# Kernel tuning notes

Hardware: AMD Instinct MI355X
Metric: run time of the kernel (lower is better)

The kernel has to match this reference:

```python
import jax, jax.numpy as jnp
import numpy as np

N, E1, E2, P, H = 4096, 131072, 131072, 65536, 128
ROLE_VOCAB, ROLE_DIM, IDX_VOCAB, IDX_DIM = 8, 16, 1024, 8


def _lin_init(key, fan_in, fan_out):
    k1, k2 = jax.random.split(key)
    bound = 1.0 / np.sqrt(fan_in)
    W = jax.random.uniform(k1, (fan_in, fan_out), jnp.float32, -bound, bound)
    b = jax.random.uniform(k2, (fan_out,), jnp.float32, -bound, bound)
    return W, b


def setup_inputs() -> dict:
    key = jax.random.key(0)
    ks = jax.random.split(key, 24)
    d = {}
    d["block_features"] = jax.random.normal(ks[0], (N, 16), jnp.float32)
    d["role_ids"] = jax.random.randint(ks[1], (N,), 0, ROLE_VOCAB)
    d["b2b_src"] = jax.random.randint(ks[2], (E1,), 0, N)
    d["b2b_dst"] = jax.random.randint(ks[3], (E1,), 0, N)
    d["b2b_w"] = jax.random.uniform(ks[4], (E1,), jnp.float32)
    d["p2b_pin"] = jax.random.randint(ks[5], (E2,), 0, P)
    d["p2b_block"] = jax.random.randint(ks[6], (E2,), 0, N)
    d["p2b_w"] = jax.random.uniform(ks[7], (E2,), jnp.float32)
    d["pins_pos"] = jax.random.normal(ks[8], (P, 2), jnp.float32)
    d["area_targets"] = jax.random.uniform(ks[9], (N,), jnp.float32)
    # parameters
    d["role_emb"] = jax.random.normal(ks[10], (ROLE_VOCAB, ROLE_DIM), jnp.float32)
    d["idx_emb"] = jax.random.normal(ks[11], (IDX_VOCAB, IDX_DIM), jnp.float32)
    d["in_W1"], d["in_b1"] = _lin_init(ks[12], 16 + IDX_DIM + ROLE_DIM, H)
    d["in_W2"], d["in_b2"] = _lin_init(ks[13], H, H)
    d["b2b_W1"], d["b2b_b1"] = _lin_init(ks[14], 2 * H + 1, H)
    d["b2b_W2"], d["b2b_b2"] = _lin_init(ks[15], H, H)
    d["p2b_W1"], d["p2b_b1"] = _lin_init(ks[16], H + 3, H)
    d["p2b_W2"], d["p2b_b2"] = _lin_init(ks[17], H, H)
    d["self_W"], d["self_b"] = _lin_init(ks[18], H, H)
    d["ln_g"] = jnp.ones((H,), jnp.float32)
    d["ln_b"] = jnp.zeros((H,), jnp.float32)
    d["gp_W1"], d["gp_b1"] = _lin_init(ks[19], 2 * H, H)
    d["gp_W2"], d["gp_b2"] = _lin_init(ks[20], H, H)
    return d


def _mlp2(x, W1, b1, W2, b2):
    return jax.nn.relu(x @ W1 + b1) @ W2 + b2


def _forward(block_features, role_ids, b2b_src, b2b_dst, b2b_w, p2b_pin, p2b_block,
             p2b_w, pins_pos, area_targets, role_emb, idx_emb, in_W1, in_b1, in_W2,
             in_b2, b2b_W1, b2b_b1, b2b_W2, b2b_b2, p2b_W1, p2b_b1, p2b_W2, p2b_b2,
             self_W, self_b, ln_g, ln_b, gp_W1, gp_b1, gp_W2, gp_b2):
    n = block_features.shape[0]
    role_e = role_emb[role_ids]                       # [N, role_dim]
    idx_e = idx_emb[jnp.arange(n) % IDX_VOCAB]        # [N, idx_dim]
    x = jnp.concatenate([block_features, role_e, idx_e], axis=-1)
    h = jax.nn.relu(_mlp2(x, in_W1, in_b1, in_W2, in_b2))  # input_proj ends in ReLU

    # --- b2b messages: two directed messages per undirected edge ---
    max_b2b = jax.lax.stop_gradient(jnp.maximum(jnp.max(jnp.abs(b2b_w)), 1.0))
    w = (b2b_w / max_b2b)[:, None]                    # [E1, 1]
    hi, hj = h[b2b_src], h[b2b_dst]                   # [E1, H]
    m_ij = _mlp2(jnp.concatenate([hi, hj, w], -1), b2b_W1, b2b_b1, b2b_W2, b2b_b2)
    m_ji = _mlp2(jnp.concatenate([hj, hi, w], -1), b2b_W1, b2b_b1, b2b_W2, b2b_b2)
    agg = jnp.zeros_like(h).at[b2b_src].add(m_ij).at[b2b_dst].add(m_ji)

    # --- p2b messages ---
    total_area = jnp.maximum(jnp.sum(area_targets), 1e-6)
    case_scale = jax.lax.stop_gradient(jnp.maximum(jnp.sqrt(total_area), 1e-6))
    max_p2b = jax.lax.stop_gradient(jnp.maximum(jnp.max(jnp.abs(p2b_w)), 1.0))
    pin_feats = jnp.concatenate(
        [pins_pos[p2b_pin] / case_scale, (p2b_w / max_p2b)[:, None]], axis=-1)  # [E2, 3]
    m_p = _mlp2(jnp.concatenate([h[p2b_block], pin_feats], -1),
                p2b_W1, p2b_b1, p2b_W2, p2b_b2)
    agg = agg.at[p2b_block].add(m_p)

    # --- combine + LayerNorm ---
    z = h @ self_W + self_b + agg
    mu = jnp.mean(z, axis=-1, keepdims=True)
    var = jnp.mean(jnp.square(z - mu), axis=-1, keepdims=True)
    block_embeddings = (z - mu) / jnp.sqrt(var + 1e-5) * ln_g + ln_b

    pooled = jnp.concatenate(
        [block_embeddings.mean(axis=0), block_embeddings.max(axis=0)], axis=-1)
    graph_embedding = _mlp2(pooled, gp_W1, gp_b1, gp_W2, gp_b2)
    return block_embeddings, graph_embedding


def reference(block_features, role_ids, b2b_src, b2b_dst, b2b_w, p2b_pin, p2b_block,
              p2b_w, pins_pos, area_targets, role_emb, idx_emb, in_W1, in_b1, in_W2,
              in_b2, b2b_W1, b2b_b1, b2b_W2, b2b_b2, p2b_W1, p2b_b1, p2b_W2, p2b_b2,
              self_W, self_b, ln_g, ln_b, gp_W1, gp_b1, gp_W2, gp_b2):
    block_embeddings, graph_embedding = _forward(
        block_features, role_ids, b2b_src, b2b_dst, b2b_w, p2b_pin, p2b_block,
        p2b_w, pins_pos, area_targets, role_emb, idx_emb, in_W1, in_b1, in_W2,
        in_b2, b2b_W1, b2b_b1, b2b_W2, b2b_b2, p2b_W1, p2b_b1, p2b_W2, p2b_b2,
        self_W, self_b, ln_g, ln_b, gp_W1, gp_b1, gp_W2, gp_b2)
    block_mask = jnp.ones((block_features.shape[0],), dtype=bool)
    return block_embeddings, graph_embedding, block_mask
```

## Files before the change

### kernel.cpp

```cpp
#include <hip/hip_runtime.h>
#include <hip/hip_bf16.h>

#define N_NODES 4096
#define HDIM    128
#define E1      131072
#define E2      131072
#define NMSG_B2B (2 * E1)
#define CAPB    192
#define CAPP    96

#define OFF_PSUM   8
#define OFF_PMAX   136
#define OFF_HB     264
#define OFF_P      (OFF_HB + 262144)
#define OFF_Q      (OFF_P + 524288)
#define OFF_R      (OFF_Q + 524288)
#define OFF_CP     (OFF_R + 524288)
#define OFF_B2H    (OFF_CP + 24576)
#define OFF_B2L    (OFF_B2H + 8192)
#define OFF_P2H    (OFF_B2L + 8192)
#define OFF_P2L    (OFF_P2H + 8192)
#define OFF_SWP    (OFF_P2L + 8192)
#define OFF_IW1    (OFF_SWP + 8192)
#define OFF_IW2    (OFF_IW1 + 4096)
#define OFF_WLAST  (OFF_IW2 + 8192)
#define OFF_PEXTRA (OFF_WLAST + 128)
#define OFF_CNTB   (OFF_PEXTRA + 384)
#define OFF_CNTP   (OFF_CNTB + 4096)
#define OFF_BKB    (OFF_CNTP + 4096)
#define OFF_BKP    (OFF_BKB + 2 * N_NODES * CAPB)
#define WS_FLOATS  (OFF_BKP + 2 * N_NODES * CAPP)

typedef short short8 __attribute__((ext_vector_type(8)));
typedef float f32x4 __attribute__((ext_vector_type(4)));

__device__ __forceinline__ unsigned short f2bf(float f) {
  union { float f; unsigned u; } v; v.f = f;
  unsigned r = v.u + 0x7fffu + ((v.u >> 16) & 1u);
  return (unsigned short)(r >> 16);
}
__device__ __forceinline__ float bf2f(unsigned short h) {
  return __uint_as_float((unsigned)h << 16);
}
__device__ __forceinline__ int il(int c) { return ((c & 63) << 1) | (c >> 6); }

__global__ __launch_bounds__(256) void setup_kernel(const float* __restrict__ b2bw,
                                                    const float* __restrict__ p2bw,
                                                    const float* __restrict__ area,
                                                    const float* __restrict__ bW1,
                                                    const float* __restrict__ bW2,
                                                    const float* __restrict__ pW1,
                                                    const float* __restrict__ pW2,
                                                    const float* __restrict__ sWm,
                                                    const float* __restrict__ iW1,
                                                    const float* __restrict__ iW2,
                                                    float* __restrict__ ws) {
  __shared__ float red[256];
  int b = blockIdx.x, t = threadIdx.x;
  if (b < 32) {
    float m = 0.f;
    for (int i = b * 256 + t; i < E1; i += 32 * 256) m = fmaxf(m, fabsf(b2bw[i]));
    red[t] = m; __syncthreads();
    for (int s = 128; s > 0; s >>= 1) { if (t < s) red[t] = fmaxf(red[t], red[t + s]); __syncthreads(); }
    if (t == 0) atomicMax((unsigned*)&ws[0], __float_as_uint(red[0]));
  } else if (b < 64) {
    float m = 0.f;
    for (int i = (b - 32) * 256 + t; i < E2; i += 32 * 256) m = fmaxf(m, fabsf(p2bw[i]));
    red[t] = m; __syncthreads();
    for (int s = 128; s > 0; s >>= 1) { if (t < s) red[t] = fmaxf(red[t], red[t + s]); __syncthreads(); }
    if (t == 0) atomicMax((unsigned*)&ws[1], __float_as_uint(red[0]));
  } else if (b < 96) {
    float s0 = 0.f;
    for (int i = (b - 64) * 256 + t; i < N_NODES; i += 32 * 256) s0 += area[i];
    red[t] = s0; __syncthreads();
    for (int s = 128; s > 0; s >>= 1) { if (t < s) red[t] += red[t + s]; __syncthreads(); }
    if (t == 0) atomicAdd(&ws[2], red[0]);
  } else if (b == 96) {
    if (t < HDIM) ((int*)ws)[OFF_PMAX + t] = 0x80000000;
    int* cB = (int*)ws + OFF_CNTB;
    for (int i = t; i < 2 * N_NODES; i += 256) cB[i] = 0;
  } else {
    unsigned short* Cp  = (unsigned short*)(ws + OFF_CP);
    unsigned short* B2h = (unsigned short*)(ws + OFF_B2H);
    unsigned short* B2l = (unsigned short*)(ws + OFF_B2L);
    unsigned short* P2h = (unsigned short*)(ws + OFF_P2H);
    unsigned short* P2l = (unsigned short*)(ws + OFF_P2L);
    unsigned short* Swp = (unsigned short*)(ws + OFF_SWP);
    unsigned short* I1p = (unsigned short*)(ws + OFF_IW1);
    unsigned short* I2p = (unsigned short*)(ws + OFF_IW2);
    float* wlast = ws + OFF_WLAST;
    float* pextra = ws + OFF_PEXTRA;
    const int total = 156160;
    for (int x = (b - 97) * 256 + t; x < total; x += 128 * 256) {
      if (x < 49152) {
        int j = x & 7, lane = (x >> 3) & 63, ks = (x >> 9) & 3, nc = x >> 11;
        int col = nc * 16 + (lane & 15), k = ks * 32 + (lane >> 4) * 8 + j;
        float v;
        if (col < 128)      v = bW1[k * 128 + col];
        else if (col < 256) v = bW1[(128 + k) * 128 + (col - 128)];
        else                v = pW1[k * 128 + (col - 256)];
        Cp[x] = f2bf(v);
      } else if (x < 114688) {
        int u = (x - 49152) & 16383, which = (x - 49152) >> 14;
        int j = u & 7, lane = (u >> 3) & 63, ks = (u >> 9) & 3, nt = u >> 11;
        int n = nt * 16 + (lane & 15), k = ks * 32 + (lane >> 4) * 8 + j;
        float v = (which < 2) ? bW2[k * 128 + n] : pW2[k * 128 + n];
        unsigned short hi = f2bf(v);
        unsigned short outv = (which & 1) ? f2bf(v - bf2f(hi)) : hi;
        ((which < 2) ? ((which & 1) ? B2l : B2h) : ((which & 1) ? P2l : P2h))[u] = outv;
      } else if (x < 131072) {
        int u = x - 114688;
        int j = u & 7, lane = (u >> 3) & 63, ks = (u >> 9) & 3, nt = u >> 11;
        int n = nt * 16 + (lane & 15), k = ks * 32 + (lane >> 4) * 8 + j;
        Swp[u] = f2bf(sWm[k * 128 + n]);
      } else if (x < 139264) {
        int u = x - 131072;
        int j = u & 7, lane = (u >> 3) & 63, ks = (u >> 9) & 1, nt = u >> 10;
        int n = nt * 16 + (lane & 15), k = ks * 32 + (lane >> 4) * 8 + j;
        I1p[u] = (k < 40) ? f2bf(iW1[k * 128 + n]) : 0;
      } else if (x < 155648) {
        int u = x - 139264;
        int j = u & 7, lane = (u >> 3) & 63, ks = (u >> 9) & 3, nt = u >> 11;
        int n = nt * 16 + (lane & 15), k = ks * 32 + (lane >> 4) * 8 + j;
        I2p[u] = f2bf(iW2[k * 128 + n]);
      } else if (x < 155776) {
        int c = x - 155648;
        wlast[il(c)] = bW1[256 * 128 + c];
      } else {
        int u = x - 155776;
        int r = u >> 7, c = u & 127;
        pextra[r * 128 + il(c)] = pW1[(128 + r) * 128 + c];
      }
    }
  }
}

__global__ __launch_bounds__(512) void mid_kernel(const int* __restrict__ src,
                                                  const int* __restrict__ dst,
                                                  const int* __restrict__ pblk,
                                                  const int* __restrict__ ppin,
                                                  const float* __restrict__ bwv,
                                                  const float* __restrict__ pwv,
                                                  const float* __restrict__ pins,
                                                  const float* __restrict__ bfeat,
                                                  const int* __restrict__ rid,
                                                  const float* __restrict__ remb,
                                                  const float* __restrict__ iemb,
                                                  const float* __restrict__ ib1,
                                                  const float* __restrict__ ib2,
                                                  const float* __restrict__ bb1,
                                                  const float* __restrict__ pb1,
                                                  float* __restrict__ ws,
                                                  unsigned short* __restrict__ hb) {
  __shared__ __attribute__((aligned(16))) unsigned short xs[16 * 72];
  __shared__ __attribute__((aligned(16))) unsigned short h1s[16 * 136];
  __shared__ __attribute__((aligned(16))) unsigned short hs[16 * 136];
  int tid = threadIdx.x;
  if (blockIdx.x < 768) {
    int i = blockIdx.x * 512 + tid;
    int* cntB = (int*)ws + OFF_CNTB;
    int* cntP = (int*)ws + OFF_CNTP;
    uint2* BKB = (uint2*)((int*)ws + OFF_BKB);
    uint2* BKP = (uint2*)((int*)ws + OFF_BKP);
    if (i < NMSG_B2B) {
      int e = i >> 1, d = i & 1;
      int tg = d ? dst[e] : src[e];
      int o  = d ? src[e] : dst[e];
      int pos = atomicAdd(&cntB[tg], 1);
      if (pos < CAPB) {
        uint2 v; v.x = (unsigned)o; v.y = __float_as_uint(bwv[e]);
        BKB[tg * CAPB + pos] = v;
      }
    } else {
      int e = i - NMSG_B2B;
      int pin = ppin[e];
      int tg = pblk[e];
      int pos = atomicAdd(&cntP[tg], 1);
      if (pos < CAPP) {
        uint2 v;
        v.x = ((unsigned)f2bf(pins[pin * 2 + 1]) << 16) | (unsigned)f2bf(pins[pin * 2]);
        v.y = __float_as_uint(pwv[e]);
        BKP[tg * CAPP + pos] = v;
      }
    }
    return;
  }
  const unsigned short* I1p = (const unsigned short*)(ws + OFF_IW1);
  const unsigned short* I2p = (const unsigned short*)(ws + OFF_IW2);
  const unsigned short* Cp  = (const unsigned short*)(ws + OFF_CP);
  float* P = ws + OFF_P;
  float* Q = ws + OFF_Q;
  float* R = ws + OFF_R;
  int n0 = (blockIdx.x - 768) * 16;
  for (int idx = tid; idx < 1024; idx += 512) {
    int m = idx >> 6, c = idx & 63;
    int n = n0 + m;
    float v = 0.f;
    if (c < 16)      v = bfeat[n * 16 + c];
    else if (c < 32) v = remb[rid[n] * 16 + (c - 16)];
    else if (c < 40) v = iemb[(n & 1023) * 8 + (c - 32)];
    xs[m * 72 + c] = f2bf(v);
  }
  __syncthreads();
  int lane = tid & 63, wv = tid >> 6;
  int l15 = lane & 15, q = lane >> 4;
  f32x4 zero = {0.f, 0.f, 0.f, 0.f};
  f32x4 a1 = zero;
#pragma unroll
  for (int ks = 0; ks < 2; ks++) {
    short8 af = *(const short8*)(&xs[l15 * 72 + ks * 32 + q * 8]);
    short8 bfr = *(const short8*)(I1p + ((wv * 2 + ks) * 64 + lane) * 8);
    a1 = __builtin_amdgcn_mfma_f32_16x16x32_bf16(af, bfr, a1, 0, 0, 0);
  }
  {
    int n = wv * 16 + l15;
    float b = ib1[n];
#pragma unroll
    for (int r = 0; r < 4; r++)
      h1s[(q * 4 + r) * 136 + n] = f2bf(fmaxf(a1[r] + b, 0.f));
  }
  __syncthreads();
  f32x4 a2 = zero;
#pragma unroll
  for (int ks = 0; ks < 4; ks++) {
    short8 af = *(const short8*)(&h1s[l15 * 136 + ks * 32 + q * 8]);
    short8 bfr = *(const short8*)(I2p + ((wv * 4 + ks) * 64 + lane) * 8);
    a2 = __builtin_amdgcn_mfma_f32_16x16x32_bf16(af, bfr, a2, 0, 0, 0);
  }
  {
    int n = wv * 16 + l15;
    float b = ib2[n];
#pragma unroll
    for (int r = 0; r < 4; r++) {
      unsigned short hv = f2bf(fmaxf(a2[r] + b, 0.f));
      hs[(q * 4 + r) * 136 + n] = hv;
      hb[(n0 + q * 4 + r) * 128 + n] = hv;
    }
  }
  __syncthreads();
  f32x4 a3[3];
#pragma unroll
  for (int i = 0; i < 3; i++) a3[i] = zero;
#pragma unroll
  for (int ks = 0; ks < 4; ks++) {
    short8 af = *(const short8*)(&hs[l15 * 136 + ks * 32 + q * 8]);
#pragma unroll
    for (int j = 0; j < 3; j++) {
      short8 bfr = *(const short8*)(Cp + (((3 * wv + j) * 4 + ks) * 64 + lane) * 8);
      a3[j] = __builtin_amdgcn_mfma_f32_16x16x32_bf16(af, bfr, a3[j], 0, 0, 0);
    }
  }
#pragma unroll
  for (int j = 0; j < 3; j++) {
    int col = (3 * wv + j) * 16 + l15;
    int arr = col >> 7, cc = col & 127;
    float bias = (arr == 0) ? bb1[cc] : ((arr == 2) ? pb1[cc] : 0.f);
    float* dstp = (arr == 0) ? P : ((arr == 1) ? Q : R);
    int ic = il(cc);
#pragma unroll
    for (int r = 0; r < 4; r++)
      dstp[(n0 + q * 4 + r) * 128 + ic] = a3[j][r] + bias;
  }
}

__global__ __launch_bounds__(1024) void fused_kernel(const unsigned short* __restrict__ hb,
                                                     const float* __restrict__ sb,
                                                     const float* __restrict__ lng,
                                                     const float* __restrict__ lnb,
                                                     const float* __restrict__ bb2,
                                                     const float* __restrict__ pb2,
                                                     const float* __restrict__ gW1,
                                                     const float* __restrict__ gb1,
                                                     const float* __restrict__ gW2,
                                                     const float* __restrict__ gb2,
                                                     float* __restrict__ ws,
                                                     float* __restrict__ out) {
  __shared__ __attribute__((aligned(16))) unsigned short A[16 * 648];
  __shared__ float partB[16][130];
  __shared__ float partP[16][130];
  __shared__ float zp[2][8 * 128];
  __shared__ float zs[8 * 133];
  __shared__ float muS[8], rsg[8];
  __shared__ float partS[8][16], partQ[8][16];
  __shared__ float psumL[8][128];
  __shared__ int   pmaxL[8][128];
  __shared__ int   isLast;
  int tid = threadIdx.x;
  int n0 = blockIdx.x * 8;
  int lane = tid & 63, wv = tid >> 6;
  const int* cntBp = (const int*)ws + OFF_CNTB;
  const int* cntPp = (const int*)ws + OFF_CNTP;
  if (tid < 128) {
    int m = tid >> 4, o = (tid & 15) * 8;
    *(uint4*)(&A[m * 648 + o]) = *(const uint4*)(hb + (n0 + m) * 128 + o);
  }
  if (tid < 648) {
    int r = tid / 81, o = (tid % 81) * 8;
    *(uint4*)(&A[(8 + r) * 648 + o]) = make_uint4(0u, 0u, 0u, 0u);
  }
  {
    const uint2* BKB = (const uint2*)((const int*)ws + OFF_BKB);
    const uint2* BKP = (const uint2*)((const int*)ws + OFF_BKP);
    const float* Pm = ws + OFF_P;
    const float* Qm = ws + OFF_Q;
    const float* Rm = ws + OFF_R;
    float invb = 1.f / fmaxf(__uint_as_float(((const unsigned*)ws)[0]), 1.f);
    float invp = 1.f / fmaxf(__uint_as_float(((const unsigned*)ws)[1]), 1.f);
    float cs = fmaxf(sqrtf(fmaxf(ws[2], 1e-6f)), 1e-6f);
    float invc = 1.f / cs;
    float2 wlr = *(const float2*)(ws + OFF_WLAST + 2 * lane);
    float2 e0r = *(const float2*)(ws + OFF_PEXTRA + 2 * lane);
    float2 e1r = *(const float2*)(ws + OFF_PEXTRA + 128 + 2 * lane);
    float2 e2r = *(const float2*)(ws + OFF_PEXTRA + 256 + 2 * lane);
    float2 wl = {invb * wlr.x, invb * wlr.y};
    float2 e0 = {invc * e0r.x, invc * e0r.y};
    float2 e1 = {invc * e1r.x, invc * e1r.y};
    float2 e2 = {invp * e2r.x, invp * e2r.y};
    int ln = wv >> 1, hf = wv & 1;
    int node = n0 + ln;
    {
      int cnt = min(cntBp[node], CAPB);
      int mh = cnt >> 1;
      int m = hf ? mh : 0;
      int me = hf ? cnt : mh;
      const uint2* bk = BKB + node * CAPB;
      float2 p = *(const float2*)(Pm + node * 128 + 2 * lane);
      float a0 = 0.f, a1 = 0.f, b0 = 0.f, b1 = 0.f;
      for (; m + 8 <= me; m += 8) {
        uint2 k0 = bk[m],     k1 = bk[m + 1], k2 = bk[m + 2], k3 = bk[m + 3];
        uint2 k4 = bk[m + 4], k5 = bk[m + 5], k6 = bk[m + 6], k7 = bk[m + 7];
        float2 q0 = *(const float2*)(Qm + k0.x * 128 + 2 * lane);
        float2 q1 = *(const float2*)(Qm + k1.x * 128 + 2 * lane);
        float2 q2 = *(const float2*)(Qm + k2.x * 128 + 2 * lane);
        float2 q3 = *(const float2*)(Qm + k3.x * 128 + 2 * lane);
        float2 q4 = *(const float2*)(Qm + k4.x * 128 + 2 * lane);
        float2 q5 = *(const float2*)(Qm + k5.x * 128 + 2 * lane);
        float2 q6 = *(const float2*)(Qm + k6.x * 128 + 2 * lane);
        float2 q7 = *(const float2*)(Qm + k7.x * 128 + 2 * lane);
        float w0 = __uint_as_float(k0.y), w1 = __uint_as_float(k1.y);
        float w2 = __uint_as_float(k2.y), w3 = __uint_as_float(k3.y);
        float w4 = __uint_as_float(k4.y), w5 = __uint_as_float(k5.y);
        float w6 = __uint_as_float(k6.y), w7 = __uint_as_float(k7.y);
        a0 += fmaxf(fmaf(w0, wl.x, p.x) + q0.x, 0.f);
        a1 += fmaxf(fmaf(w0, wl.y, p.y) + q0.y, 0.f);
        b0 += fmaxf(fmaf(w1, wl.x, p.x) + q1.x, 0.f);
        b1 += fmaxf(fmaf(w1, wl.y, p.y) + q1.y, 0.f);
        a0 += fmaxf(fmaf(w2, wl.x, p.x) + q2.x, 0.f);
        a1 += fmaxf(fmaf(w2, wl.y, p.y) + q2.y, 0.f);
        b0 += fmaxf(fmaf(w3, wl.x, p.x) + q3.x, 0.f);
        b1 += fmaxf(fmaf(w3, wl.y, p.y) + q3.y, 0.f);
        a0 += fmaxf(fmaf(w4, wl.x, p.x) + q4.x, 0.f);
        a1 += fmaxf(fmaf(w4, wl.y, p.y) + q4.y, 0.f);
        b0 += fmaxf(fmaf(w5, wl.x, p.x) + q5.x, 0.f);
        b1 += fmaxf(fmaf(w5, wl.y, p.y) + q5.y, 0.f);
        a0 += fmaxf(fmaf(w6, wl.x, p.x) + q6.x, 0.f);
        a1 += fmaxf(fmaf(w6, wl.y, p.y) + q6.y, 0.f);
        b0 += fmaxf(fmaf(w7, wl.x, p.x) + q7.x, 0.f);
        b1 += fmaxf(fmaf(w7, wl.y, p.y) + q7.y, 0.f);
      }
      for (; m < me; m++) {
        uint2 k0 = bk[m];
        float w0 = __uint_as_float(k0.y);
        float2 q0 = *(const float2*)(Qm + k0.x * 128 + 2 * lane);
        a0 += fmaxf(fmaf(w0, wl.x, p.x) + q0.x, 0.f);
        a1 += fmaxf(fmaf(w0, wl.y, p.y) + q0.y, 0.f);
      }
      partB[wv][lane]      = a0 + b0;
      partB[wv][64 + lane] = a1 + b1;
    }
    {
      int cnt = min(cntPp[node], CAPP);
      int mh = cnt >> 1;
      int m = hf ? mh : 0;
      int me = hf ? cnt : mh;
      const uint2* bk = BKP + node * CAPP;
      float2 r = *(const float2*)(Rm + node * 128 + 2 * lane);
      float a0 = 0.f, a1 = 0.f, b0 = 0.f, b1 = 0.f;
      for (; m + 4 <= me; m += 4) {
        uint2 k0 = bk[m], k1 = bk[m + 1], k2 = bk[m + 2], k3 = bk[m + 3];
        float x00 = __uint_as_float((k0.x & 0xFFFFu) << 16);
        float x01 = __uint_as_float(k0.x & 0xFFFF0000u);
        float x02 = __uint_as_float(k0.y);
        float x10 = __uint_as_float((k1.x & 0xFFFFu) << 16);
        float x11 = __uint_as_float(k1.x & 0xFFFF0000u);
        float x12 = __uint_as_float(k1.y);
        float x20 = __uint_as_float((k2.x & 0xFFFFu) << 16);
        float x21 = __uint_as_float(k2.x & 0xFFFF0000u);
        float x22 = __uint_as_float(k2.y);
        float x30 = __uint_as_float((k3.x & 0xFFFFu) << 16);
        float x31 = __uint_as_float(k3.x & 0xFFFF0000u);
        float x32 = __uint_as_float(k3.y);
        a0 += fmaxf(fmaf(x02, e2.x, fmaf(x01, e1.x, fmaf(x00, e0.x, r.x))), 0.f);
        a1 += fmaxf(fmaf(x02, e2.y, fmaf(x01, e1.y, fmaf(x00, e0.y, r.y))), 0.f);
        b0 += fmaxf(fmaf(x12, e2.x, fmaf(x11, e1.x, fmaf(x10, e0.x, r.x))), 0.f);
        b1 += fmaxf(fmaf(x12, e2.y, fmaf(x11, e1.y, fmaf(x10, e0.y, r.y))), 0.f);
        a0 += fmaxf(fmaf(x22, e2.x, fmaf(x21, e1.x, fmaf(x20, e0.x, r.x))), 0.f);
        a1 += fmaxf(fmaf(x22, e2.y, fmaf(x21, e1.y, fmaf(x20, e0.y, r.y))), 0.f);
        b0 += fmaxf(fmaf(x32, e2.x, fmaf(x31, e1.x, fmaf(x30, e0.x, r.x))), 0.f);
        b1 += fmaxf(fmaf(x32, e2.y, fmaf(x31, e1.y, fmaf(x30, e0.y, r.y))), 0.f);
      }
      for (; m < me; m++) {
        uint2 k0 = bk[m];
        float x00 = __uint_as_float((k0.x & 0xFFFFu) << 16);
        float x01 = __uint_as_float(k0.x & 0xFFFF0000u);
        float x02 = __uint_as_float(k0.y);
        a0 += fmaxf(fmaf(x02, e2.x, fmaf(x01, e1.x, fmaf(x00, e0.x, r.x))), 0.f);
        a1 += fmaxf(fmaf(x02, e2.y, fmaf(x01, e1.y, fmaf(x00, e0.y, r.y))), 0.f);
      }
      partP[wv][lane]      = a0 + b0;
      partP[wv][64 + lane] = a1 + b1;
    }
  }
  __syncthreads();
  {
    int r = tid >> 7, c = tid & 127;
    float sb_ = partB[2 * r][c] + partB[2 * r + 1][c];
    float sp_ = partP[2 * r][c] + partP[2 * r + 1][c];
    unsigned short h0 = f2bf(sb_);
    A[r * 648 + 128 + c] = h0;
    A[r * 648 + 256 + c] = f2bf(sb_ - bf2f(h0));
    unsigned short h1v = f2bf(sp_);
    A[r * 648 + 384 + c] = h1v;
    A[r * 648 + 512 + c] = f2bf(sp_ - bf2f(h1v));
  }
  __syncthreads();
  int l15 = lane & 15, q = lane >> 4;
  int ct = wv & 7, half = wv >> 3;
  f32x4 zero = {0.f, 0.f, 0.f, 0.f};
  f32x4 acc = zero;
  const unsigned short* bufs[7] = {
    (const unsigned short*)(ws + OFF_SWP), (const unsigned short*)(ws + OFF_B2H),
    (const unsigned short*)(ws + OFF_B2L), (const unsigned short*)(ws + OFF_B2H),
    (const unsigned short*)(ws + OFF_P2H), (const unsigned short*)(ws + OFF_P2L),
    (const unsigned short*)(ws + OFF_P2H)};
  const int segs[7] = {0, 128, 128, 256, 384, 384, 512};
  int p0 = half ? 4 : 0, p1 = half ? 7 : 4;
  for (int p = p0; p < p1; p++) {
#pragma unroll
    for (int ks = 0; ks < 4; ks++) {
      short8 af = *(const short8*)(&A[l15 * 648 + segs[p] + ks * 32 + q * 8]);
      short8 bfr = *(const short8*)(bufs[p] + ((ct * 4 + ks) * 64 + lane) * 8);
      acc = __builtin_amdgcn_mfma_f32_16x16x32_bf16(af, bfr, acc, 0, 0, 0);
    }
  }
  if (q < 2) {
    int nn = ct * 16 + l15;
#pragma unroll
    for (int r = 0; r < 4; r++)
      zp[half][(q * 4 + r) * 128 + nn] = acc[r];
  }
  __syncthreads();
  {
    int row = tid >> 7, c = tid & 127;
    float cb = (float)cntBp[n0 + row], cp = (float)cntPp[n0 + row];
    zs[row * 133 + c] = zp[0][row * 128 + c] + zp[1][row * 128 + c]
                      + sb[c] + cb * bb2[c] + cp * pb2[c];
  }
  __syncthreads();
  if (tid < 128) {
    int r = tid >> 4, g = tid & 15;
    const float* zr = &zs[r * 133 + g * 8];
    float s = 0.f, s2 = 0.f;
#pragma unroll
    for (int i = 0; i < 8; i++) { float v = zr[i]; s += v; s2 += v * v; }
    partS[r][g] = s; partQ[r][g] = s2;
  }
  __syncthreads();
  if (tid < 8) {
    float s = 0.f, s2 = 0.f;
#pragma unroll
    for (int g = 0; g < 16; g++) { s += partS[tid][g]; s2 += partQ[tid][g]; }
    float m = s * (1.f / 128.f);
    float var = s2 * (1.f / 128.f) - m * m;
    muS[tid] = m;
    rsg[tid] = rsqrtf(fmaxf(var, 0.f) + 1e-5f);
  }
  __syncthreads();
  {
    int row = tid >> 7, c = tid & 127;
    float g = lng[c], b = lnb[c];
    float v = (zs[row * 133 + c] - muS[row]) * rsg[row] * g + b;
    out[(n0 + row) * 128 + c] = v;
    psumL[row][c] = v;
    int e = __float_as_int(v);
    e = e >= 0 ? e : (e ^ 0x7fffffff);
    pmaxL[row][c] = e;
  }
  __syncthreads();
  if (tid < 128) {
    float s = 0.f; int mx = 0x80000000;
#pragma unroll
    for (int g = 0; g < 8; g++) { s += psumL[g][tid]; mx = max(mx, pmaxL[g][tid]); }
    atomicAdd(&ws[OFF_PSUM + tid], s);
    atomicMax(&((int*)ws)[OFF_PMAX + tid], mx);
  }
  if (tid < 8) out[N_NODES * HDIM + HDIM + n0 + tid] = 1.0f;
  __syncthreads();
  if (tid == 0) {
    __threadfence();
    int v = atomicAdd(&((int*)ws)[3], 1);
    isLast = (v == (int)gridDim.x - 1);
  }
  __syncthreads();
  if (!isLast) return;
  __shared__ float pooled[256];
  __shared__ float gpart[8][128];
  __shared__ float g1[128];
  if (tid < 128) {
    pooled[tid] = atomicAdd(&ws[OFF_PSUM + tid], 0.f) * (1.f / (float)N_NODES);
  } else if (tid < 256) {
    int e = atomicAdd(&((int*)ws)[OFF_PMAX + (tid - 128)], 0);
    int bits = e >= 0 ? e : (e ^ 0x7fffffff);
    pooled[tid] = __int_as_float(bits);
  }
  __syncthreads();
  {
    int c = tid & 127, g = tid >> 7;
    float acc2 = 0.f;
#pragma unroll 8
    for (int k = g * 32; k < g * 32 + 32; k++) acc2 += pooled[k] * gW1[k * 128 + c];
    gpart[g][c] = acc2;
  }
  __syncthreads();
  if (tid < 128) {
    float s = gb1[tid];
#pragma unroll
    for (int g = 0; g < 8; g++) s += gpart[g][tid];
    g1[tid] = fmaxf(s, 0.f);
  }
  __syncthreads();
  {
    int c = tid & 127, g = tid >> 7;
    float acc2 = 0.f;
#pragma unroll 8
    for (int k = g * 16; k < g * 16 + 16; k++) acc2 += g1[k] * gW2[k * 128 + c];
    gpart[g][c] = acc2;
  }
  __syncthreads();
  if (tid < 128) {
    float s = gb2[tid];
#pragma unroll
    for (int g = 0; g < 8; g++) s += gpart[g][tid];
    out[N_NODES * HDIM + tid] = s;
  }
}

extern "C" void kernel_launch(void* const* d_in, const int* in_sizes, int n_in,
                              void* d_out, int out_size, void* d_ws, size_t ws_size,
                              hipStream_t stream) {
  const float* bfeat = (const float*)d_in[0];
  const int*   rid   = (const int*)d_in[1];
  const int*   bsrc  = (const int*)d_in[2];
  const int*   bdst  = (const int*)d_in[3];
  const float* bw    = (const float*)d_in[4];
  const int*   ppin  = (const int*)d_in[5];
  const int*   pblk  = (const int*)d_in[6];
  const float* pw    = (const float*)d_in[7];
  const float* pins  = (const float*)d_in[8];
  const float* area  = (const float*)d_in[9];
  const float* remb  = (const float*)d_in[10];
  const float* iemb  = (const float*)d_in[11];
  const float* inW1  = (const float*)d_in[12];
  const float* inb1  = (const float*)d_in[13];
  const float* inW2  = (const float*)d_in[14];
  const float* inb2  = (const float*)d_in[15];
  const float* bW1   = (const float*)d_in[16];
  const float* bb1   = (const float*)d_in[17];
  const float* bW2   = (const float*)d_in[18];
  const float* bb2   = (const float*)d_in[19];
  const float* pW1   = (const float*)d_in[20];
  const float* pb1   = (const float*)d_in[21];
  const float* pW2   = (const float*)d_in[22];
  const float* pb2   = (const float*)d_in[23];
  const float* sW    = (const float*)d_in[24];
  const float* sb    = (const float*)d_in[25];
  const float* lng   = (const float*)d_in[26];
  const float* lnb   = (const float*)d_in[27];
  const float* gW1   = (const float*)d_in[28];
  const float* gb1   = (const float*)d_in[29];
  const float* gW2   = (const float*)d_in[30];
  const float* gb2   = (const float*)d_in[31];

  float* ws  = (float*)d_ws;
  float* out = (float*)d_out;
  unsigned short* hb = (unsigned short*)(ws + OFF_HB);

  hipMemsetAsync(d_ws, 0, 264 * sizeof(float), stream);
  setup_kernel<<<225, 256, 0, stream>>>(bw, pw, area,
                                        bW1, bW2, pW1, pW2, sW, inW1, inW2, ws);
  mid_kernel<<<1024, 512, 0, stream>>>(bsrc, bdst, pblk, ppin, bw, pw, pins,
                                       bfeat, rid, remb, iemb, inb1, inb2, bb1, pb1,
                                       ws, hb);
  fused_kernel<<<512, 1024, 0, stream>>>(hb, sb, lng, lnb, bb2, pb2,
                                         gW1, gb1, gW2, gb2, ws, out);
}
```

Baseline: 204.9 us.

## Split edge aggregation into separate kernel and use full 16-row MFMA tiles

Moves the per-node edge message gather/aggregation out of the fused kernel into a new edge_kernel that writes split-bf16 aggregates to a workspace buffer. The fused kernel then processes 16 nodes per block instead of 8, filling all 16 rows of the MFMA tile instead of zero-padding half of it, which halves the number of blocks and wasted matrix work. The cost is an extra kernel launch and a round trip of the aggregates through global memory.

```diff
diff --git a/kernel.cpp b/kernel.cpp
--- a/kernel.cpp
+++ b/kernel.cpp
@@ -29,7 +29,8 @@
 #define OFF_CNTP   (OFF_CNTB + 4096)
 #define OFF_BKB    (OFF_CNTP + 4096)
 #define OFF_BKP    (OFF_BKB + 2 * N_NODES * CAPB)
-#define WS_FLOATS  (OFF_BKP + 2 * N_NODES * CAPP)
+#define OFF_SB     (OFF_BKP + 2 * N_NODES * CAPP)
+#define WS_FLOATS  (OFF_SB + 524288)
 
 typedef short short8 __attribute__((ext_vector_type(8)));
 typedef float f32x4 __attribute__((ext_vector_type(4)));
@@ -263,6 +264,140 @@
   }
 }
 
+__global__ __launch_bounds__(512) void edge_kernel(float* __restrict__ ws) {
+  __shared__ float partB[8][130];
+  __shared__ float partP[8][130];
+  int tid = threadIdx.x;
+  int lane = tid & 63, wv = tid >> 6;
+  int n0 = blockIdx.x * 4;
+  const int* cntBp = (const int*)ws + OFF_CNTB;
+  const int* cntPp = (const int*)ws + OFF_CNTP;
+  const uint2* BKB = (const uint2*)((const int*)ws + OFF_BKB);
+  const uint2* BKP = (const uint2*)((const int*)ws + OFF_BKP);
+  const float* Pm = ws + OFF_P;
+  const float* Qm = ws + OFF_Q;
+  const float* Rm = ws + OFF_R;
+  float invb = 1.f / fmaxf(__uint_as_float(((const unsigned*)ws)[0]), 1.f);
+  float invp = 1.f / fmaxf(__uint_as_float(((const unsigned*)ws)[1]), 1.f);
+  float cs = fmaxf(sqrtf(fmaxf(ws[2], 1e-6f)), 1e-6f);
+  float invc = 1.f / cs;
+  float2 wlr = *(const float2*)(ws + OFF_WLAST + 2 * lane);
+  float2 e0r = *(const float2*)(ws + OFF_PEXTRA + 2 * lane);
+  float2 e1r = *(const float2*)(ws + OFF_PEXTRA + 128 + 2 * lane);
+  float2 e2r = *(const float2*)(ws + OFF_PEXTRA + 256 + 2 * lane);
+  float2 wl = {invb * wlr.x, invb * wlr.y};
+  float2 e0 = {invc * e0r.x, invc * e0r.y};
+  float2 e1 = {invc * e1r.x, invc * e1r.y};
+  float2 e2 = {invp * e2r.x, invp * e2r.y};
+  int ln = wv >> 1, hf = wv & 1;
+  int node = n0 + ln;
+  {
+    int cnt = min(cntBp[node], CAPB);
+    int mh = cnt >> 1;
+    int m = hf ? mh : 0;
+    int me = hf ? cnt : mh;
+    const uint2* bk = BKB + node * CAPB;
+    float2 p = *(const float2*)(Pm + node * 128 + 2 * lane);
+    float a0 = 0.f, a1 = 0.f, b0 = 0.f, b1 = 0.f;
+    for (; m + 8 <= me; m += 8) {
+      uint2 k0 = bk[m],     k1 = bk[m + 1], k2 = bk[m + 2], k3 = bk[m + 3];
+      uint2 k4 = bk[m + 4], k5 = bk[m + 5], k6 = bk[m + 6], k7 = bk[m + 7];
+      float2 q0 = *(const float2*)(Qm + k0.x * 128 + 2 * lane);
+      float2 q1 = *(const float2*)(Qm + k1.x * 128 + 2 * lane);
+      float2 q2 = *(const float2*)(Qm + k2.x * 128 + 2 * lane);
+      float2 q3 = *(const float2*)(Qm + k3.x * 128 + 2 * lane);
+      float2 q4 = *(const float2*)(Qm + k4.x * 128 + 2 * lane);
+      float2 q5 = *(const float2*)(Qm + k5.x * 128 + 2 * lane);
+      float2 q6 = *(const float2*)(Qm + k6.x * 128 + 2 * lane);
+      float2 q7 = *(const float2*)(Qm + k7.x * 128 + 2 * lane);
+      float w0 = __uint_as_float(k0.y), w1 = __uint_as_float(k1.y);
+      float w2 = __uint_as_float(k2.y), w3 = __uint_as_float(k3.y);
+      float w4 = __uint_as_float(k4.y), w5 = __uint_as_float(k5.y);
+      float w6 = __uint_as_float(k6.y), w7 = __uint_as_float(k7.y);
+      a0 += fmaxf(fmaf(w0, wl.x, p.x) + q0.x, 0.f);
+      a1 += fmaxf(fmaf(w0, wl.y, p.y) + q0.y, 0.f);
+      b0 += fmaxf(fmaf(w1, wl.x, p.x) + q1.x, 0.f);
+      b1 += fmaxf(fmaf(w1, wl.y, p.y) + q1.y, 0.f);
+      a0 += fmaxf(fmaf(w2, wl.x, p.x) + q2.x, 0.f);
+      a1 += fmaxf(fmaf(w2, wl.y, p.y) + q2.y, 0.f);
+      b0 += fmaxf(fmaf(w3, wl.x, p.x) + q3.x, 0.f);
+      b1 += fmaxf(fmaf(w3, wl.y, p.y) + q3.y, 0.f);
+      a0 += fmaxf(fmaf(w4, wl.x, p.x) + q4.x, 0.f);
+      a1 += fmaxf(fmaf(w4, wl.y, p.y) + q4.y, 0.f);
+      b0 += fmaxf(fmaf(w5, wl.x, p.x) + q5.x, 0.f);
+      b1 += fmaxf(fmaf(w5, wl.y, p.y) + q5.y, 0.f);
+      a0 += fmaxf(fmaf(w6, wl.x, p.x) + q6.x, 0.f);
+      a1 += fmaxf(fmaf(w6, wl.y, p.y) + q6.y, 0.f);
+      b0 += fmaxf(fmaf(w7, wl.x, p.x) + q7.x, 0.f);
+      b1 += fmaxf(fmaf(w7, wl.y, p.y) + q7.y, 0.f);
+    }
+    for (; m < me; m++) {
+      uint2 k0 = bk[m];
+      float w0 = __uint_as_float(k0.y);
+      float2 q0 = *(const float2*)(Qm + k0.x * 128 + 2 * lane);
+      a0 += fmaxf(fmaf(w0, wl.x, p.x) + q0.x, 0.f);
+      a1 += fmaxf(fmaf(w0, wl.y, p.y) + q0.y, 0.f);
+    }
+    partB[wv][lane]      = a0 + b0;
+    partB[wv][64 + lane] = a1 + b1;
+  }
+  {
+    int cnt = min(cntPp[node], CAPP);
+    int mh = cnt >> 1;
+    int m = hf ? mh : 0;
+    int me = hf ? cnt : mh;
+    const uint2* bk = BKP + node * CAPP;
+    float2 r = *(const float2*)(Rm + node * 128 + 2 * lane);
+    float a0 = 0.f, a1 = 0.f, b0 = 0.f, b1 = 0.f;
+    for (; m + 4 <= me; m += 4) {
+      uint2 k0 = bk[m], k1 = bk[m + 1], k2 = bk[m + 2], k3 = bk[m + 3];
+      float x00 = __uint_as_float((k0.x & 0xFFFFu) << 16);
+      float x01 = __uint_as_float(k0.x & 0xFFFF0000u);
+      float x02 = __uint_as_float(k0.y);
+      float x10 = __uint_as_float((k1.x & 0xFFFFu) << 16);
+      float x11 = __uint_as_float(k1.x & 0xFFFF0000u);
+      float x12 = __uint_as_float(k1.y);
+      float x20 = __uint_as_float((k2.x & 0xFFFFu) << 16);
+      float x21 = __uint_as_float(k2.x & 0xFFFF0000u);
+      float x22 = __uint_as_float(k2.y);
+      float x30 = __uint_as_float((k3.x & 0xFFFFu) << 16);
+      float x31 = __uint_as_float(k3.x & 0xFFFF0000u);
+      float x32 = __uint_as_float(k3.y);
+      a0 += fmaxf(fmaf(x02, e2.x, fmaf(x01, e1.x, fmaf(x00, e0.x, r.x))), 0.f);
+      a1 += fmaxf(fmaf(x02, e2.y, fmaf(x01, e1.y, fmaf(x00, e0.y, r.y))), 0.f);
+      b0 += fmaxf(fmaf(x12, e2.x, fmaf(x11, e1.x, fmaf(x10, e0.x, r.x))), 0.f);
+      b1 += fmaxf(fmaf(x12, e2.y, fmaf(x11, e1.y, fmaf(x10, e0.y, r.y))), 0.f);
+      a0 += fmaxf(fmaf(x22, e2.x, fmaf(x21, e1.x, fmaf(x20, e0.x, r.x))), 0.f);
+      a1 += fmaxf(fmaf(x22, e2.y, fmaf(x21, e1.y, fmaf(x20, e0.y, r.y))), 0.f);
+      b0 += fmaxf(fmaf(x32, e2.x, fmaf(x31, e1.x, fmaf(x30, e0.x, r.x))), 0.f);
+      b1 += fmaxf(fmaf(x32, e2.y, fmaf(x31, e1.y, fmaf(x30, e0.y, r.y))), 0.f);
+    }
+    for (; m < me; m++) {
+      uint2 k0 = bk[m];
+      float x00 = __uint_as_float((k0.x & 0xFFFFu) << 16);
+      float x01 = __uint_as_float(k0.x & 0xFFFF0000u);
+      float x02 = __uint_as_float(k0.y);
+      a0 += fmaxf(fmaf(x02, e2.x, fmaf(x01, e1.x, fmaf(x00, e0.x, r.x))), 0.f);
+      a1 += fmaxf(fmaf(x02, e2.y, fmaf(x01, e1.y, fmaf(x00, e0.y, r.y))), 0.f);
+    }
+    partP[wv][lane]      = a0 + b0;
+    partP[wv][64 + lane] = a1 + b1;
+  }
+  __syncthreads();
+  {
+    int r = tid >> 7, c = tid & 127;
+    float sb_ = partB[2 * r][c] + partB[2 * r + 1][c];
+    float sp_ = partP[2 * r][c] + partP[2 * r + 1][c];
+    unsigned short* SBp = (unsigned short*)(ws + OFF_SB) + (size_t)(n0 + r) * 512;
+    unsigned short h0 = f2bf(sb_);
+    SBp[c]       = h0;
+    SBp[128 + c] = f2bf(sb_ - bf2f(h0));
+    unsigned short h1v = f2bf(sp_);
+    SBp[256 + c] = h1v;
+    SBp[384 + c] = f2bf(sp_ - bf2f(h1v));
+  }
+}
+
 __global__ __launch_bounds__(1024) void fused_kernel(const unsigned short* __restrict__ hb,
                                                      const float* __restrict__ sb,
                                                      const float* __restrict__ lng,
@@ -276,152 +411,24 @@
                                                      float* __restrict__ ws,
                                                      float* __restrict__ out) {
   __shared__ __attribute__((aligned(16))) unsigned short A[16 * 648];
-  __shared__ float partB[16][130];
-  __shared__ float partP[16][130];
-  __shared__ float zp[2][8 * 128];
-  __shared__ float zs[8 * 133];
-  __shared__ float muS[8], rsg[8];
-  __shared__ float partS[8][16], partQ[8][16];
+  __shared__ float zp[2][16 * 128];
+  __shared__ float zs[16 * 133];
+  __shared__ float muS[16], rsg[16];
+  __shared__ float partS[16][16], partQ[16][16];
   __shared__ float psumL[8][128];
   __shared__ int   pmaxL[8][128];
   __shared__ int   isLast;
   int tid = threadIdx.x;
-  int n0 = blockIdx.x * 8;
+  int n0 = blockIdx.x * 16;
   int lane = tid & 63, wv = tid >> 6;
-  const int* cntBp = (const int*)ws + OFF_CNTB;
-  const int* cntPp = (const int*)ws + OFF_CNTP;
-  if (tid < 128) {
+  if (tid < 256) {
     int m = tid >> 4, o = (tid & 15) * 8;
     *(uint4*)(&A[m * 648 + o]) = *(const uint4*)(hb + (n0 + m) * 128 + o);
   }
-  if (tid < 648) {
-    int r = tid / 81, o = (tid % 81) * 8;
-    *(uint4*)(&A[(8 + r) * 648 + o]) = make_uint4(0u, 0u, 0u, 0u);
-  }
-  {
-    const uint2* BKB = (const uint2*)((const int*)ws + OFF_BKB);
-    const uint2* BKP = (const uint2*)((const int*)ws + OFF_BKP);
-    const float* Pm = ws + OFF_P;
-    const float* Qm = ws + OFF_Q;
-    const float* Rm = ws + OFF_R;
-    float invb = 1.f / fmaxf(__uint_as_float(((const unsigned*)ws)[0]), 1.f);
-    float invp = 1.f / fmaxf(__uint_as_float(((const unsigned*)ws)[1]), 1.f);
-    float cs = fmaxf(sqrtf(fmaxf(ws[2], 1e-6f)), 1e-6f);
-    float invc = 1.f / cs;
-    float2 wlr = *(const float2*)(ws + OFF_WLAST + 2 * lane);
-    float2 e0r = *(const float2*)(ws + OFF_PEXTRA + 2 * lane);
-    float2 e1r = *(const float2*)(ws + OFF_PEXTRA + 128 + 2 * lane);
-    float2 e2r = *(const float2*)(ws + OFF_PEXTRA + 256 + 2 * lane);
-    float2 wl = {invb * wlr.x, invb * wlr.y};
-    float2 e0 = {invc * e0r.x, invc * e0r.y};
-    float2 e1 = {invc * e1r.x, invc * e1r.y};
-    float2 e2 = {invp * e2r.x, invp * e2r.y};
-    int ln = wv >> 1, hf = wv & 1;
-    int node = n0 + ln;
-    {
-      int cnt = min(cntBp[node], CAPB);
-      int mh = cnt >> 1;
-      int m = hf ? mh : 0;
-      int me = hf ? cnt : mh;
-      const uint2* bk = BKB + node * CAPB;
-      float2 p = *(const float2*)(Pm + node * 128 + 2 * lane);
-      float a0 = 0.f, a1 = 0.f, b0 = 0.f, b1 = 0.f;
-      for (; m + 8 <= me; m += 8) {
-        uint2 k0 = bk[m],     k1 = bk[m + 1], k2 = bk[m + 2], k3 = bk[m + 3];
-        uint2 k4 = bk[m + 4], k5 = bk[m + 5], k6 = bk[m + 6], k7 = bk[m + 7];
-        float2 q0 = *(const float2*)(Qm + k0.x * 128 + 2 * lane);
-        float2 q1 = *(const float2*)(Qm + k1.x * 128 + 2 * lane);
-        float2 q2 = *(const float2*)(Qm + k2.x * 128 + 2 * lane);
-        float2 q3 = *(const float2*)(Qm + k3.x * 128 + 2 * lane);
-        float2 q4 = *(const float2*)(Qm + k4.x * 128 + 2 * lane);
-        float2 q5 = *(const float2*)(Qm + k5.x * 128 + 2 * lane);
-        float2 q6 = *(const float2*)(Qm + k6.x * 128 + 2 * lane);
-        float2 q7 = *(const float2*)(Qm + k7.x * 128 + 2 * lane);
-        float w0 = __uint_as_float(k0.y), w1 = __uint_as_float(k1.y);
-        float w2 = __uint_as_float(k2.y), w3 = __uint_as_float(k3.y);
-        float w4 = __uint_as_float(k4.y), w5 = __uint_as_float(k5.y);
-        float w6 = __uint_as_float(k6.y), w7 = __uint_as_float(k7.y);
-        a0 += fmaxf(fmaf(w0, wl.x, p.x) + q0.x, 0.f);
-        a1 += fmaxf(fmaf(w0, wl.y, p.y) + q0.y, 0.f);
-        b0 += fmaxf(fmaf(w1, wl.x, p.x) + q1.x, 0.f);
-        b1 += fmaxf(fmaf(w1, wl.y, p.y) + q1.y, 0.f);
-        a0 += fmaxf(fmaf(w2, wl.x, p.x) + q2.x, 0.f);
-        a1 += fmaxf(fmaf(w2, wl.y, p.y) + q2.y, 0.f);
-        b0 += fmaxf(fmaf(w3, wl.x, p.x) + q3.x, 0.f);
-        b1 += fmaxf(fmaf(w3, wl.y, p.y) + q3.y, 0.f);
-        a0 += fmaxf(fmaf(w4, wl.x, p.x) + q4.x, 0.f);
-        a1 += fmaxf(fmaf(w4, wl.y, p.y) + q4.y, 0.f);
-        b0 += fmaxf(fmaf(w5, wl.x, p.x) + q5.x, 0.f);
-        b1 += fmaxf(fmaf(w5, wl.y, p.y) + q5.y, 0.f);
-        a0 += fmaxf(fmaf(w6, wl.x, p.x) + q6.x, 0.f);
-        a1 += fmaxf(fmaf(w6, wl.y, p.y) + q6.y, 0.f);
-        b0 += fmaxf(fmaf(w7, wl.x, p.x) + q7.x, 0.f);
-        b1 += fmaxf(fmaf(w7, wl.y, p.y) + q7.y, 0.f);
-      }
-      for (; m < me; m++) {
-        uint2 k0 = bk[m];
-        float w0 = __uint_as_float(k0.y);
-        float2 q0 = *(const float2*)(Qm + k0.x * 128 + 2 * lane);
-        a0 += fmaxf(fmaf(w0, wl.x, p.x) + q0.x, 0.f);
-        a1 += fmaxf(fmaf(w0, wl.y, p.y) + q0.y, 0.f);
-      }
-      partB[wv][lane]      = a0 + b0;
-      partB[wv][64 + lane] = a1 + b1;
-    }
-    {
-      int cnt = min(cntPp[node], CAPP);
-      int mh = cnt >> 1;
-      int m = hf ? mh : 0;
-      int me = hf ? cnt : mh;
-      const uint2* bk = BKP + node * CAPP;
-      float2 r = *(const float2*)(Rm + node * 128 + 2 * lane);
-      float a0 = 0.f, a1 = 0.f, b0 = 0.f, b1 = 0.f;
-      for (; m + 4 <= me; m += 4) {
-        uint2 k0 = bk[m], k1 = bk[m + 1], k2 = bk[m + 2], k3 = bk[m + 3];
-        float x00 = __uint_as_float((k0.x & 0xFFFFu) << 16);
-        float x01 = __uint_as_float(k0.x & 0xFFFF0000u);
-        float x02 = __uint_as_float(k0.y);
-        float x10 = __uint_as_float((k1.x & 0xFFFFu) << 16);
-        float x11 = __uint_as_float(k1.x & 0xFFFF0000u);
-        float x12 = __uint_as_float(k1.y);
-        float x20 = __uint_as_float((k2.x & 0xFFFFu) << 16);
-        float x21 = __uint_as_float(k2.x & 0xFFFF0000u);
-        float x22 = __uint_as_float(k2.y);
-        float x30 = __uint_as_float((k3.x & 0xFFFFu) << 16);
-        float x31 = __uint_as_float(k3.x & 0xFFFF0000u);
-        float x32 = __uint_as_float(k3.y);
-        a0 += fmaxf(fmaf(x02, e2.x, fmaf(x01, e1.x, fmaf(x00, e0.x, r.x))), 0.f);
-        a1 += fmaxf(fmaf(x02, e2.y, fmaf(x01, e1.y, fmaf(x00, e0.y, r.y))), 0.f);
-        b0 += fmaxf(fmaf(x12, e2.x, fmaf(x11, e1.x, fmaf(x10, e0.x, r.x))), 0.f);
-        b1 += fmaxf(fmaf(x12, e2.y, fmaf(x11, e1.y, fmaf(x10, e0.y, r.y))), 0.f);
-        a0 += fmaxf(fmaf(x22, e2.x, fmaf(x21, e1.x, fmaf(x20, e0.x, r.x))), 0.f);
-        a1 += fmaxf(fmaf(x22, e2.y, fmaf(x21, e1.y, fmaf(x20, e0.y, r.y))), 0.f);
-        b0 += fmaxf(fmaf(x32, e2.x, fmaf(x31, e1.x, fmaf(x30, e0.x, r.x))), 0.f);
-        b1 += fmaxf(fmaf(x32, e2.y, fmaf(x31, e1.y, fmaf(x30, e0.y, r.y))), 0.f);
-      }
-      for (; m < me; m++) {
-        uint2 k0 = bk[m];
-        float x00 = __uint_as_float((k0.x & 0xFFFFu) << 16);
-        float x01 = __uint_as_float(k0.x & 0xFFFF0000u);
-        float x02 = __uint_as_float(k0.y);
-        a0 += fmaxf(fmaf(x02, e2.x, fmaf(x01, e1.x, fmaf(x00, e0.x, r.x))), 0.f);
-        a1 += fmaxf(fmaf(x02, e2.y, fmaf(x01, e1.y, fmaf(x00, e0.y, r.y))), 0.f);
-      }
-      partP[wv][lane]      = a0 + b0;
-      partP[wv][64 + lane] = a1 + b1;
-    }
-  }
-  __syncthreads();
-  {
-    int r = tid >> 7, c = tid & 127;
-    float sb_ = partB[2 * r][c] + partB[2 * r + 1][c];
-    float sp_ = partP[2 * r][c] + partP[2 * r + 1][c];
-    unsigned short h0 = f2bf(sb_);
-    A[r * 648 + 128 + c] = h0;
-    A[r * 648 + 256 + c] = f2bf(sb_ - bf2f(h0));
-    unsigned short h1v = f2bf(sp_);
-    A[r * 648 + 384 + c] = h1v;
-    A[r * 648 + 512 + c] = f2bf(sp_ - bf2f(h1v));
+  {
+    const unsigned short* SBp = (const unsigned short*)(ws + OFF_SB);
+    int m = tid >> 6, o = (tid & 63) * 8;
+    *(uint4*)(&A[m * 648 + 128 + o]) = *(const uint4*)(SBp + (size_t)(n0 + m) * 512 + o);
   }
   __syncthreads();
   int l15 = lane & 15, q = lane >> 4;
@@ -443,21 +450,26 @@
       acc = __builtin_amdgcn_mfma_f32_16x16x32_bf16(af, bfr, acc, 0, 0, 0);
     }
   }
-  if (q < 2) {
+  {
     int nn = ct * 16 + l15;
 #pragma unroll
     for (int r = 0; r < 4; r++)
       zp[half][(q * 4 + r) * 128 + nn] = acc[r];
   }
   __syncthreads();
-  {
-    int row = tid >> 7, c = tid & 127;
-    float cb = (float)cntBp[n0 + row], cp = (float)cntPp[n0 + row];
-    zs[row * 133 + c] = zp[0][row * 128 + c] + zp[1][row * 128 + c]
-                      + sb[c] + cb * bb2[c] + cp * pb2[c];
-  }
-  __syncthreads();
-  if (tid < 128) {
+  const int* cntB = (const int*)ws + OFF_CNTB;
+  const int* cntP = (const int*)ws + OFF_CNTP;
+  {
+    int idx = tid;
+    for (int rep = 0; rep < 2; rep++, idx += 1024) {
+      int row = idx >> 7, c = idx & 127;
+      float cb = (float)cntB[n0 + row], cp = (float)cntP[n0 + row];
+      zs[row * 133 + c] = zp[0][row * 128 + c] + zp[1][row * 128 + c]
+                        + sb[c] + cb * bb2[c] + cp * pb2[c];
+    }
+  }
+  __syncthreads();
+  if (tid < 256) {
     int r = tid >> 4, g = tid & 15;
     const float* zr = &zs[r * 133 + g * 8];
     float s = 0.f, s2 = 0.f;
@@ -466,7 +478,7 @@
     partS[r][g] = s; partQ[r][g] = s2;
   }
   __syncthreads();
-  if (tid < 8) {
+  if (tid < 16) {
     float s = 0.f, s2 = 0.f;
 #pragma unroll
     for (int g = 0; g < 16; g++) { s += partS[tid][g]; s2 += partQ[tid][g]; }
@@ -477,14 +489,18 @@
   }
   __syncthreads();
   {
-    int row = tid >> 7, c = tid & 127;
+    int c = tid & 127, grp = tid >> 7;
     float g = lng[c], b = lnb[c];
-    float v = (zs[row * 133 + c] - muS[row]) * rsg[row] * g + b;
-    out[(n0 + row) * 128 + c] = v;
-    psumL[row][c] = v;
-    int e = __float_as_int(v);
-    e = e >= 0 ? e : (e ^ 0x7fffffff);
-    pmaxL[row][c] = e;
+    float ls = 0.f; int lm = 0x80000000;
+    for (int r = grp * 2; r < grp * 2 + 2; r++) {
+      float v = (zs[r * 133 + c] - muS[r]) * rsg[r] * g + b;
+      out[(n0 + r) * 128 + c] = v;
+      ls += v;
+      int e = __float_as_int(v);
+      e = e >= 0 ? e : (e ^ 0x7fffffff);
+      lm = max(lm, e);
+    }
+    psumL[grp][c] = ls; pmaxL[grp][c] = lm;
   }
   __syncthreads();
   if (tid < 128) {
@@ -494,7 +510,7 @@
     atomicAdd(&ws[OFF_PSUM + tid], s);
     atomicMax(&((int*)ws)[OFF_PMAX + tid], mx);
   }
-  if (tid < 8) out[N_NODES * HDIM + HDIM + n0 + tid] = 1.0f;
+  if (tid < 16) out[N_NODES * HDIM + HDIM + n0 + tid] = 1.0f;
   __syncthreads();
   if (tid == 0) {
     __threadfence();
@@ -591,6 +607,7 @@
   mid_kernel<<<1024, 512, 0, stream>>>(bsrc, bdst, pblk, ppin, bw, pw, pins,
                                        bfeat, rid, remb, iemb, inb1, inb2, bb1, pb1,
                                        ws, hb);
-  fused_kernel<<<512, 1024, 0, stream>>>(hb, sb, lng, lnb, bb2, pb2,
+  edge_kernel<<<1024, 512, 0, stream>>>(ws);
+  fused_kernel<<<256, 1024, 0, stream>>>(hb, sb, lng, lnb, bb2, pb2,
                                          gW1, gb1, gW2, gb2, ws, out);
 }
```

After: 201.8 us. About the same (-1.5%).
